# Kernel tuning notes

Hardware: AMD Instinct MI355X
Metric: run time of the kernel (lower is better)

Reference implementation:

```python
import jax, jax.numpy as jnp
import numpy as np

MARGIN = 0.3
EPS = 1e-12


def setup_inputs() -> dict:
    key = jax.random.key(0)
    k1, k2 = jax.random.split(key)
    n, d = 4096, 1024
    inputs = jax.random.normal(k1, (n, d), dtype=jnp.float32)
    targets = jax.random.randint(k2, (n,), 0, 64, dtype=jnp.int64)
    return {"inputs": inputs, "targets": targets}


def reference(inputs, targets):
    n = inputs.shape[0]
    # pairwise Euclidean distance matrix: ||xi||^2 + ||xj||^2 - 2 xi.xj
    sq = jnp.sum(inputs * inputs, axis=1)  # [n]
    dist2 = sq[:, None] + sq[None, :] - 2.0 * (inputs @ inputs.T)
    dist = jnp.sqrt(jnp.clip(dist2, EPS))  # [n, n]
    # same-label mask (includes diagonal, matching original)
    mask = targets[:, None] == targets[None, :]
    # fused masked row-wise hard mining
    neg_inf = jnp.asarray(-jnp.inf, dist.dtype)
    pos_inf = jnp.asarray(jnp.inf, dist.dtype)
    dist_ap = jnp.max(jnp.where(mask, dist, neg_inf), axis=1)  # hardest positive
    dist_an = jnp.min(jnp.where(mask, pos_inf, dist), axis=1)  # hardest negative
    # MarginRankingLoss with y=1: mean(relu(margin - (dist_an - dist_ap)))
    loss = jnp.mean(jnp.maximum(MARGIN - (dist_an - dist_ap), 0.0))
    prec = jnp.sum((dist_an > dist_ap).astype(jnp.float32)) / n
    return (loss, prec)
```

## Files before the change

### kernel.cpp

```cpp
#include <hip/hip_runtime.h>
#include <stdint.h>

#define MARGIN 0.3f
#define EPS 1e-12f

typedef __attribute__((ext_vector_type(8))) __bf16 bf16x8;
typedef __attribute__((ext_vector_type(4))) float f32x4;

__device__ __forceinline__ unsigned short f2bf(float f) {
    unsigned u = __float_as_uint(f);
    unsigned r = (u + 0x7FFFu + ((u >> 16) & 1u)) >> 16;
    return (unsigned short)r;
}

#define GLD16(gp, lp)                                                     \
    __builtin_amdgcn_global_load_lds(                                     \
        (const __attribute__((address_space(1))) void*)(gp),              \
        (__attribute__((address_space(3))) void*)(lp), 16, 0, 0)

__global__ __launch_bounds__(256) void prep_kernel(
    const float* __restrict__ X, unsigned short* __restrict__ Xbf,
    float* __restrict__ sqg, unsigned* __restrict__ apb,
    unsigned* __restrict__ anb, unsigned* __restrict__ ctr, int d) {
    const int wave = threadIdx.x >> 6, lane = threadIdx.x & 63;
    const int row = blockIdx.x * 4 + wave;
    const float4* Xr = (const float4*)(X + (size_t)row * d);
    ushort4* Or = (ushort4*)(Xbf + (size_t)row * d);
    float s = 0.0f;
    const int nq = d >> 2;
    for (int i = lane; i < nq; i += 64) {
        float4 v = Xr[i];
        s += v.x * v.x + v.y * v.y + v.z * v.z + v.w * v.w;
        ushort4 o;
        o.x = f2bf(v.x); o.y = f2bf(v.y); o.z = f2bf(v.z); o.w = f2bf(v.w);
        Or[i] = o;
    }
    for (int off = 32; off > 0; off >>= 1) s += __shfl_down(s, off, 64);
    if (lane == 0) {
        sqg[row] = s;
        apb[row] = 0u;
        anb[row] = 0x7F800000u;
    }
    if (blockIdx.x == 0 && threadIdx.x == 0) ctr[0] = 0u;
}

#define BM 256
#define BN 128
#define BK 32

__global__ __launch_bounds__(512, 4) void tri_gemm(
    const unsigned short* __restrict__ Xbf, const float* __restrict__ sqg,
    const int* __restrict__ tgt, unsigned* __restrict__ apb,
    unsigned* __restrict__ anb, unsigned* __restrict__ ctr,
    float* __restrict__ out, int n, int d, int nblk) {
    __shared__ unsigned short ldsA[2][BM * BK];
    __shared__ unsigned short ldsB[2][BN * BK];

    const int tid  = threadIdx.x;
    const int lane = tid & 63;
    const int wave = tid >> 6;
    const int wm = wave >> 1;
    const int wn = wave & 1;
    const int lo = lane & 15, hi = lane >> 4;

    const int orig = blockIdx.x;
    const int q = nblk >> 3, r = nblk & 7;
    const int xcd = orig & 7, idx = orig >> 3;
    const int bid = (xcd < r ? xcd * (q + 1) : r * (q + 1) + (xcd - r) * q) + idx;

    int bi = (int)((sqrtf(4.0f * (float)bid + 1.0f) - 1.0f) * 0.5f);
    while ((bi + 1) * (bi + 2) <= bid) ++bi;
    while (bi * (bi + 1) > bid) --bi;
    const int bj = bid - bi * (bi + 1);
    const int rowBase = bi * BM;
    const int colBase = bj * BN;

    const int lrow = lane >> 2;
    const int lk   = (lane & 3) * 8;
    const unsigned short* gA0 = Xbf + (size_t)(rowBase + wave * 16 + lrow) * d + lk;
    const unsigned short* gA1 = gA0 + (size_t)128 * d;
    const unsigned short* gB0 = Xbf + (size_t)(colBase + wave * 16 + lrow) * d + lk;

#define STAGE(bufi, k0)                                                   \
    do {                                                                  \
        GLD16(gA0 + (k0), &ldsA[bufi][wave * 512]);                       \
        GLD16(gA1 + (k0), &ldsA[bufi][(8 + wave) * 512]);                 \
        GLD16(gB0 + (k0), &ldsB[bufi][wave * 512]);                       \
    } while (0)

    f32x4 acc[4][4] = {};

    const int nt = d / BK;
    int cur = 0;
    STAGE(0, 0);
    for (int t = 0; t < nt; ++t) {
        if (t + 1 < nt) {
            STAGE(cur ^ 1, (t + 1) * BK);
            asm volatile("s_waitcnt vmcnt(3)" ::: "memory");
        } else {
            asm volatile("s_waitcnt vmcnt(0)" ::: "memory");
        }
        asm volatile("s_barrier" ::: "memory");
        bf16x8 a[4], b[4];
#pragma unroll
        for (int mi = 0; mi < 4; ++mi)
            a[mi] = *(const bf16x8*)&ldsA[cur][(wm * 64 + mi * 16 + lo) * BK + hi * 8];
#pragma unroll
        for (int ni = 0; ni < 4; ++ni)
            b[ni] = *(const bf16x8*)&ldsB[cur][(wn * 64 + ni * 16 + lo) * BK + hi * 8];
#pragma unroll
        for (int mi = 0; mi < 4; ++mi)
#pragma unroll
            for (int ni = 0; ni < 4; ++ni)
                acc[mi][ni] = __builtin_amdgcn_mfma_f32_16x16x32_bf16(
                    a[mi], b[ni], acc[mi][ni], 0, 0, 0);
        asm volatile("s_barrier" ::: "memory");
        cur ^= 1;
    }

    float sqj[4];
    int   tj[4];
#pragma unroll
    for (int ni = 0; ni < 4; ++ni) {
        const int gj = colBase + wn * 64 + ni * 16 + lo;
        sqj[ni] = sqg[gj];
        tj[ni]  = tgt[gj];
    }
    float cap[4], can[4];
#pragma unroll
    for (int ni = 0; ni < 4; ++ni) { cap[ni] = 0.0f; can[ni] = __uint_as_float(0x7F800000u); }

#pragma unroll
    for (int mi = 0; mi < 4; ++mi) {
#pragma unroll
        for (int j = 0; j < 4; ++j) {
            const int gi = rowBase + wm * 64 + mi * 16 + hi * 4 + j;
            const float sqi = sqg[gi];
            const int   ti  = tgt[gi];
            float ap = 0.0f;
            float an = __uint_as_float(0x7F800000u);
#pragma unroll
            for (int ni = 0; ni < 4; ++ni) {
                const float d2 = sqi + sqj[ni] - 2.0f * acc[mi][ni][j];
                const float dist = sqrtf(fmaxf(d2, EPS));
                if (ti == tj[ni]) {
                    ap = fmaxf(ap, dist);
                    cap[ni] = fmaxf(cap[ni], dist);
                } else {
                    an = fminf(an, dist);
                    can[ni] = fminf(can[ni], dist);
                }
            }
#pragma unroll
            for (int m = 1; m < 16; m <<= 1) {
                ap = fmaxf(ap, __shfl_xor(ap, m, 64));
                an = fminf(an, __shfl_xor(an, m, 64));
            }
            if (lo == 0) {
                atomicMax(&apb[gi], __float_as_uint(ap));
                atomicMin(&anb[gi], __float_as_uint(an));
            }
        }
    }
#pragma unroll
    for (int ni = 0; ni < 4; ++ni) {
        float ap = cap[ni], an = can[ni];
#pragma unroll
        for (int m = 16; m < 64; m <<= 1) {
            ap = fmaxf(ap, __shfl_xor(ap, m, 64));
            an = fminf(an, __shfl_xor(an, m, 64));
        }
        if (hi == 0) {
            const int gj = colBase + wn * 64 + ni * 16 + lo;
            atomicMax(&apb[gj], __float_as_uint(ap));
            atomicMin(&anb[gj], __float_as_uint(an));
        }
    }

    __threadfence();
    __syncthreads();
    __shared__ int lastFlag;
    if (tid == 0) {
        unsigned prev = __hip_atomic_fetch_add(ctr, 1u, __ATOMIC_ACQ_REL,
                                               __HIP_MEMORY_SCOPE_AGENT);
        lastFlag = (prev == (unsigned)(nblk - 1)) ? 1 : 0;
    }
    __syncthreads();
    if (lastFlag) {
        float ls = 0.0f, pc = 0.0f;
        for (int i = tid; i < n; i += 512) {
            const float ap = __uint_as_float(__hip_atomic_load(
                &apb[i], __ATOMIC_RELAXED, __HIP_MEMORY_SCOPE_AGENT));
            const float an = __uint_as_float(__hip_atomic_load(
                &anb[i], __ATOMIC_RELAXED, __HIP_MEMORY_SCOPE_AGENT));
            ls += fmaxf(MARGIN - (an - ap), 0.0f);
            pc += (an > ap) ? 1.0f : 0.0f;
        }
        __shared__ float rl[8], rp[8];
        for (int off = 32; off > 0; off >>= 1) {
            ls += __shfl_down(ls, off, 64);
            pc += __shfl_down(pc, off, 64);
        }
        if ((tid & 63) == 0) { rl[tid >> 6] = ls; rp[tid >> 6] = pc; }
        __syncthreads();
        if (tid == 0) {
            float L = 0.0f, P = 0.0f;
#pragma unroll
            for (int w = 0; w < 8; ++w) { L += rl[w]; P += rp[w]; }
            out[0] = L / (float)n;
            out[1] = P / (float)n;
        }
    }
}

__global__ __launch_bounds__(256) void fb_zero(float* __restrict__ out) {
    if (threadIdx.x == 0) { out[0] = 0.0f; out[1] = 0.0f; }
}

__global__ __launch_bounds__(256) void fb_row(
    const float* __restrict__ X, const int* __restrict__ tgt,
    float* __restrict__ out, int n, int d) {
    __shared__ float xi[4096];
    const int i = blockIdx.x;
    const int tid = threadIdx.x;
    for (int k = tid; k < d; k += 256) xi[k] = X[(size_t)i * d + k];
    __syncthreads();
    const int ti = tgt[i];
    float ap = 0.0f;
    float an = __uint_as_float(0x7F800000u);
    for (int j = tid; j < n; j += 256) {
        const float4* Xj = (const float4*)(X + (size_t)j * d);
        float s = 0.0f;
        for (int k4 = 0; k4 < (d >> 2); ++k4) {
            float4 v = Xj[k4];
            float4 u = *(const float4*)&xi[k4 * 4];
            float dx = u.x - v.x, dy = u.y - v.y, dz = u.z - v.z, dw = u.w - v.w;
            s += dx * dx + dy * dy + dz * dz + dw * dw;
        }
        const float dist = sqrtf(fmaxf(s, EPS));
        if (tgt[j] == ti) ap = fmaxf(ap, dist);
        else              an = fminf(an, dist);
    }
    for (int m = 1; m < 64; m <<= 1) {
        ap = fmaxf(ap, __shfl_xor(ap, m, 64));
        an = fminf(an, __shfl_xor(an, m, 64));
    }
    __shared__ float rap[4], ran[4];
    const int wave = tid >> 6, lane = tid & 63;
    if (lane == 0) { rap[wave] = ap; ran[wave] = an; }
    __syncthreads();
    if (tid == 0) {
        ap = fmaxf(fmaxf(rap[0], rap[1]), fmaxf(rap[2], rap[3]));
        an = fminf(fminf(ran[0], ran[1]), fminf(ran[2], ran[3]));
        atomicAdd(&out[0], fmaxf(MARGIN - (an - ap), 0.0f));
        atomicAdd(&out[1], (an > ap) ? 1.0f : 0.0f);
    }
}

__global__ __launch_bounds__(64) void fb_scale(float* __restrict__ out, float inv_n) {
    if (threadIdx.x == 0) { out[0] *= inv_n; out[1] *= inv_n; }
}

extern "C" void kernel_launch(void* const* d_in, const int* in_sizes, int n_in,
                              void* d_out, int out_size, void* d_ws, size_t ws_size,
                              hipStream_t stream) {
    const float* X   = (const float*)d_in[0];
    const int*   tgt = (const int*)d_in[1];
    const int n = in_sizes[1];
    const int d = in_sizes[0] / n;

    const size_t need = (size_t)n * d * 2 + (size_t)n * 4 * 3 + 4;
    if (ws_size >= need && (n % BM) == 0 && (d % (2 * BK)) == 0) {
        char* ws = (char*)d_ws;
        unsigned short* Xbf = (unsigned short*)ws;
        float*    sqg = (float*)(ws + (size_t)n * d * 2);
        unsigned* apb = (unsigned*)((char*)sqg + (size_t)n * 4);
        unsigned* anb = apb + n;
        unsigned* ctr = anb + n;

        const int nbI = n / BM;
        const int nblk = nbI * (nbI + 1);
        prep_kernel<<<n / 4, 256, 0, stream>>>(X, Xbf, sqg, apb, anb, ctr, d);
        tri_gemm<<<nblk, 512, 0, stream>>>(Xbf, sqg, tgt, apb, anb, ctr,
                                           (float*)d_out, n, d, nblk);
    } else {
        fb_zero<<<1, 256, 0, stream>>>((float*)d_out);
        fb_row<<<n, 256, 0, stream>>>(X, tgt, (float*)d_out, n, d);
        fb_scale<<<1, 64, 0, stream>>>((float*)d_out, 1.0f / (float)n);
    }
}
```

Baseline: 142.7 us.

## Compute full Gram matrix with 256x256x64 tiles instead of triangular symmetric tiles

Replaces the symmetric triangular tiling (256x128 tiles that update both row and column mins/maxes) with a full square grid of 256x256 tiles and BK=64. Only row-wise reductions remain, which removes the column reduction and its atomics. The trade is roughly double the GEMM FLOPs in exchange for larger tiles, simpler indexing, fewer barriers per K step and more data reuse. The grid drops to 256 blocks and occupancy is lowered to 2 blocks per CU.

```diff
diff --git a/kernel.cpp b/kernel.cpp
--- a/kernel.cpp
+++ b/kernel.cpp
@@ -45,10 +45,10 @@
 }
 
 #define BM 256
-#define BN 128
-#define BK 32
-
-__global__ __launch_bounds__(512, 4) void tri_gemm(
+#define BN 256
+#define BK 64
+
+__global__ __launch_bounds__(512, 2) void gram_gemm(
     const unsigned short* __restrict__ Xbf, const float* __restrict__ sqg,
     const int* __restrict__ tgt, unsigned* __restrict__ apb,
     unsigned* __restrict__ anb, unsigned* __restrict__ ctr,
@@ -59,62 +59,64 @@
     const int tid  = threadIdx.x;
     const int lane = tid & 63;
     const int wave = tid >> 6;
-    const int wm = wave >> 1;
-    const int wn = wave & 1;
+    const int wm = wave >> 2;
+    const int wn = wave & 3;
     const int lo = lane & 15, hi = lane >> 4;
 
     const int orig = blockIdx.x;
-    const int q = nblk >> 3, r = nblk & 7;
-    const int xcd = orig & 7, idx = orig >> 3;
-    const int bid = (xcd < r ? xcd * (q + 1) : r * (q + 1) + (xcd - r) * q) + idx;
-
-    int bi = (int)((sqrtf(4.0f * (float)bid + 1.0f) - 1.0f) * 0.5f);
-    while ((bi + 1) * (bi + 2) <= bid) ++bi;
-    while (bi * (bi + 1) > bid) --bi;
-    const int bj = bid - bi * (bi + 1);
+    const int bid = (orig & 7) * 32 + (orig >> 3);
+    const int bi = bid >> 4, bj = bid & 15;
     const int rowBase = bi * BM;
     const int colBase = bj * BN;
 
-    const int lrow = lane >> 2;
-    const int lk   = (lane & 3) * 8;
-    const unsigned short* gA0 = Xbf + (size_t)(rowBase + wave * 16 + lrow) * d + lk;
-    const unsigned short* gA1 = gA0 + (size_t)128 * d;
-    const unsigned short* gB0 = Xbf + (size_t)(colBase + wave * 16 + lrow) * d + lk;
+    const int srow = lane >> 3;
+    const int sk   = (lane & 7) * 8;
+    const unsigned short* gA[4];
+    const unsigned short* gB[4];
+#pragma unroll
+    for (int c = 0; c < 4; ++c) {
+        const int rr = wave * 32 + c * 8 + srow;
+        gA[c] = Xbf + (size_t)(rowBase + rr) * d + sk;
+        gB[c] = Xbf + (size_t)(colBase + rr) * d + sk;
+    }
 
 #define STAGE(bufi, k0)                                                   \
     do {                                                                  \
-        GLD16(gA0 + (k0), &ldsA[bufi][wave * 512]);                       \
-        GLD16(gA1 + (k0), &ldsA[bufi][(8 + wave) * 512]);                 \
-        GLD16(gB0 + (k0), &ldsB[bufi][wave * 512]);                       \
+        _Pragma("unroll")                                                 \
+        for (int c = 0; c < 4; ++c) {                                     \
+            GLD16(gA[c] + (k0), &ldsA[bufi][(wave * 32 + c * 8) * BK]);   \
+            GLD16(gB[c] + (k0), &ldsB[bufi][(wave * 32 + c * 8) * BK]);   \
+        }                                                                 \
     } while (0)
 
-    f32x4 acc[4][4] = {};
+    f32x4 acc[8][4] = {};
 
     const int nt = d / BK;
     int cur = 0;
     STAGE(0, 0);
+    __syncthreads();
+
     for (int t = 0; t < nt; ++t) {
-        if (t + 1 < nt) {
-            STAGE(cur ^ 1, (t + 1) * BK);
-            asm volatile("s_waitcnt vmcnt(3)" ::: "memory");
-        } else {
-            asm volatile("s_waitcnt vmcnt(0)" ::: "memory");
-        }
-        asm volatile("s_barrier" ::: "memory");
-        bf16x8 a[4], b[4];
-#pragma unroll
-        for (int mi = 0; mi < 4; ++mi)
-            a[mi] = *(const bf16x8*)&ldsA[cur][(wm * 64 + mi * 16 + lo) * BK + hi * 8];
-#pragma unroll
-        for (int ni = 0; ni < 4; ++ni)
-            b[ni] = *(const bf16x8*)&ldsB[cur][(wn * 64 + ni * 16 + lo) * BK + hi * 8];
-#pragma unroll
-        for (int mi = 0; mi < 4; ++mi)
+        if (t + 1 < nt) STAGE(cur ^ 1, (t + 1) * BK);
+#pragma unroll
+        for (int kk = 0; kk < 2; ++kk) {
+            bf16x8 a[8], b[4];
+#pragma unroll
+            for (int mi = 0; mi < 8; ++mi)
+                a[mi] = *(const bf16x8*)
+                    &ldsA[cur][(wm * 128 + mi * 16 + lo) * BK + kk * 32 + hi * 8];
 #pragma unroll
             for (int ni = 0; ni < 4; ++ni)
-                acc[mi][ni] = __builtin_amdgcn_mfma_f32_16x16x32_bf16(
-                    a[mi], b[ni], acc[mi][ni], 0, 0, 0);
-        asm volatile("s_barrier" ::: "memory");
+                b[ni] = *(const bf16x8*)
+                    &ldsB[cur][(wn * 64 + ni * 16 + lo) * BK + kk * 32 + hi * 8];
+#pragma unroll
+            for (int mi = 0; mi < 8; ++mi)
+#pragma unroll
+                for (int ni = 0; ni < 4; ++ni)
+                    acc[mi][ni] = __builtin_amdgcn_mfma_f32_16x16x32_bf16(
+                        a[mi], b[ni], acc[mi][ni], 0, 0, 0);
+        }
+        __syncthreads();
         cur ^= 1;
     }
 
@@ -126,15 +128,11 @@
         sqj[ni] = sqg[gj];
         tj[ni]  = tgt[gj];
     }
-    float cap[4], can[4];
-#pragma unroll
-    for (int ni = 0; ni < 4; ++ni) { cap[ni] = 0.0f; can[ni] = __uint_as_float(0x7F800000u); }
-
-#pragma unroll
-    for (int mi = 0; mi < 4; ++mi) {
+#pragma unroll
+    for (int mi = 0; mi < 8; ++mi) {
 #pragma unroll
         for (int j = 0; j < 4; ++j) {
-            const int gi = rowBase + wm * 64 + mi * 16 + hi * 4 + j;
+            const int gi = rowBase + wm * 128 + mi * 16 + hi * 4 + j;
             const float sqi = sqg[gi];
             const int   ti  = tgt[gi];
             float ap = 0.0f;
@@ -143,13 +141,8 @@
             for (int ni = 0; ni < 4; ++ni) {
                 const float d2 = sqi + sqj[ni] - 2.0f * acc[mi][ni][j];
                 const float dist = sqrtf(fmaxf(d2, EPS));
-                if (ti == tj[ni]) {
-                    ap = fmaxf(ap, dist);
-                    cap[ni] = fmaxf(cap[ni], dist);
-                } else {
-                    an = fminf(an, dist);
-                    can[ni] = fminf(can[ni], dist);
-                }
+                if (ti == tj[ni]) ap = fmaxf(ap, dist);
+                else              an = fminf(an, dist);
             }
 #pragma unroll
             for (int m = 1; m < 16; m <<= 1) {
@@ -160,20 +153,6 @@
                 atomicMax(&apb[gi], __float_as_uint(ap));
                 atomicMin(&anb[gi], __float_as_uint(an));
             }
-        }
-    }
-#pragma unroll
-    for (int ni = 0; ni < 4; ++ni) {
-        float ap = cap[ni], an = can[ni];
-#pragma unroll
-        for (int m = 16; m < 64; m <<= 1) {
-            ap = fmaxf(ap, __shfl_xor(ap, m, 64));
-            an = fminf(an, __shfl_xor(an, m, 64));
-        }
-        if (hi == 0) {
-            const int gj = colBase + wn * 64 + ni * 16 + lo;
-            atomicMax(&apb[gj], __float_as_uint(ap));
-            atomicMin(&anb[gj], __float_as_uint(an));
         }
     }
 
@@ -270,7 +249,8 @@
     const int d = in_sizes[0] / n;
 
     const size_t need = (size_t)n * d * 2 + (size_t)n * 4 * 3 + 4;
-    if (ws_size >= need && (n % BM) == 0 && (d % (2 * BK)) == 0) {
+    if (ws_size >= need && (n % BM) == 0 && (d % BK) == 0 &&
+        ((n / BM) % 8 == 0 || (n / BM) * (n / BM) % 8 == 0)) {
         char* ws = (char*)d_ws;
         unsigned short* Xbf = (unsigned short*)ws;
         float*    sqg = (float*)(ws + (size_t)n * d * 2);
@@ -278,11 +258,11 @@
         unsigned* anb = apb + n;
         unsigned* ctr = anb + n;
 
-        const int nbI = n / BM;
-        const int nblk = nbI * (nbI + 1);
+        const int nb = n / BM;
+        const int nblk = nb * nb;
         prep_kernel<<<n / 4, 256, 0, stream>>>(X, Xbf, sqg, apb, anb, ctr, d);
-        tri_gemm<<<nblk, 512, 0, stream>>>(Xbf, sqg, tgt, apb, anb, ctr,
-                                           (float*)d_out, n, d, nblk);
+        gram_gemm<<<nblk, 512, 0, stream>>>(Xbf, sqg, tgt, apb, anb, ctr,
+                                            (float*)d_out, n, d, nblk);
     } else {
         fb_zero<<<1, 256, 0, stream>>>((float*)d_out);
         fb_row<<<n, 256, 0, stream>>>(X, tgt, (float*)d_out, n, d);
```

Measured after the change: 159.5 us. +11.8%, slower.
